# Kernel tuning notes

Hardware: AMD Instinct MI355X
Metric: run time of the kernel (lower is better)

## Reference

```python
import jax, jax.numpy as jnp
import numpy as np

B, H, S, D = 4, 16, 2048, 64
TEMPERATURE = 8.0  # sqrt(D)
MASK_FILL = -1e9


def setup_inputs() -> dict:
    key = jax.random.key(0)
    kq, kk, kv, km = jax.random.split(key, 4)
    q = jax.random.normal(kq, (B, H, S, D), dtype=jnp.float32)
    k = jax.random.normal(kk, (B, H, S, D), dtype=jnp.float32)
    v = jax.random.normal(kv, (B, H, S, D), dtype=jnp.float32)
    mask = jax.random.randint(km, (B, 1, 1, S), 0, 2, dtype=jnp.int32)
    return {"q": q, "k": k, "v": v, "mask": mask}


def reference(q, k, v, mask):
    # attn = (q / temperature) @ k^T  -> [B,H,S,S]
    attn = jnp.einsum('bhqd,bhkd->bhqk', q / TEMPERATURE, k)
    # mask-fill where mask == 0 (broadcasts over heads/query dim)
    attn = jnp.where(mask == 0, MASK_FILL, attn)
    # dropout is identity at inference (training=None in the original)
    # NOTE: the original module applies NO softmax; faithful reproduction.
    output = jnp.einsum('bhqk,bhkd->bhqd', attn, v)
    return (output, attn)
```

## Files before the change

kernel.cpp:

```cpp
#include <hip/hip_runtime.h>

constexpr int Bn = 4, Hn = 16, Sn = 2048, Dn = 64;
constexpr float MASK_FILL = -1e9f;

typedef __bf16 bf16x8 __attribute__((ext_vector_type(8)));
typedef __bf16 bf16x4 __attribute__((ext_vector_type(4)));
typedef float  f32x4  __attribute__((ext_vector_type(4)));

#define KSTRIDE 72
#define VSTRIDE 136

__global__ __launch_bounds__(256, 2) void attn_fused(
    const float* __restrict__ qg, const float* __restrict__ kg,
    const float* __restrict__ vg, const int* __restrict__ maskg,
    float* __restrict__ outg, float* __restrict__ attng)
{
  __shared__ __align__(16) __bf16 lds_k [128 * KSTRIDE];
  __shared__ __align__(16) __bf16 lds_vt[ 64 * VSTRIDE];
  __shared__ __align__(16) __bf16 lds_qs[128 * KSTRIDE];
  __shared__ int lds_m[128];

  const int qt   = blockIdx.x;
  const int bh   = blockIdx.y;
  const int b    = bh >> 4;
  const int tid  = threadIdx.x;
  const int wave = tid >> 6;
  const int lane = tid & 63;
  const int quad = lane >> 4;
  const int l16  = lane & 15;

  const size_t hbase = (size_t)bh * Sn * Dn;
  const float* qp = qg + hbase + (size_t)qt * 128 * Dn;
  float* attnp = attng + (size_t)bh * Sn * Sn + (size_t)qt * 128 * (size_t)Sn;

  {
    const int r0 = tid >> 4;
    const int c  = (tid & 15) << 2;
#pragma unroll
    for (int i = 0; i < 8; ++i) {
      const int r = r0 + (i << 4);
      f32x4 val = __builtin_nontemporal_load((const f32x4*)(qp + r * Dn + c));
      bf16x4 pk;
      pk.x = (__bf16)(val.x * 0.125f);
      pk.y = (__bf16)(val.y * 0.125f);
      pk.z = (__bf16)(val.z * 0.125f);
      pk.w = (__bf16)(val.w * 0.125f);
      *(bf16x4*)&lds_qs[r * KSTRIDE + c] = pk;
    }
  }
  __syncthreads();

  bf16x8 qa[2][2];
#pragma unroll
  for (int qs = 0; qs < 2; ++qs)
#pragma unroll
    for (int ks = 0; ks < 2; ++ks)
      qa[qs][ks] = *(const bf16x8*)&lds_qs[(wave * 32 + qs * 16 + l16) * KSTRIDE + ks * 32 + quad * 8];

  __bf16* sbuf = &lds_qs[wave * 32 * KSTRIDE];

  f32x4 oacc[2][4];
#pragma unroll
  for (int qs = 0; qs < 2; ++qs)
#pragma unroll
    for (int ds = 0; ds < 4; ++ds)
      oacc[qs][ds] = (f32x4){0.f, 0.f, 0.f, 0.f};

  for (int kt = 0; kt < 16; ++kt) {
    __syncthreads();

    {
      const int r0 = tid >> 4;
      const int c  = (tid & 15) << 2;
      const float* kp = kg + hbase + (size_t)(kt * 128) * Dn;
      const float* vp = vg + hbase + (size_t)(kt * 128) * Dn;
#pragma unroll
      for (int i = 0; i < 8; ++i) {
        const int r = r0 + (i << 4);
        f32x4 kv = *(const f32x4*)(kp + r * Dn + c);
        bf16x4 pk;
        pk.x = (__bf16)kv.x; pk.y = (__bf16)kv.y;
        pk.z = (__bf16)kv.z; pk.w = (__bf16)kv.w;
        *(bf16x4*)&lds_k[r * KSTRIDE + c] = pk;
        f32x4 vv = *(const f32x4*)(vp + r * Dn + c);
        lds_vt[(c + 0) * VSTRIDE + r] = (__bf16)vv.x;
        lds_vt[(c + 1) * VSTRIDE + r] = (__bf16)vv.y;
        lds_vt[(c + 2) * VSTRIDE + r] = (__bf16)vv.z;
        lds_vt[(c + 3) * VSTRIDE + r] = (__bf16)vv.w;
      }
      if (tid < 128) lds_m[tid] = maskg[b * Sn + kt * 128 + tid];
    }
    __syncthreads();

    f32x4 sacc[2][8];
#pragma unroll
    for (int ns = 0; ns < 8; ++ns) {
      bf16x8 kb0 = *(const bf16x8*)&lds_k[(ns * 16 + l16) * KSTRIDE +      quad * 8];
      bf16x8 kb1 = *(const bf16x8*)&lds_k[(ns * 16 + l16) * KSTRIDE + 32 + quad * 8];
#pragma unroll
      for (int qs = 0; qs < 2; ++qs) {
        f32x4 acc = (f32x4){0.f, 0.f, 0.f, 0.f};
        acc = __builtin_amdgcn_mfma_f32_16x16x32_bf16(qa[qs][0], kb0, acc, 0, 0, 0);
        acc = __builtin_amdgcn_mfma_f32_16x16x32_bf16(qa[qs][1], kb1, acc, 0, 0, 0);
        sacc[qs][ns] = acc;
      }
    }

#pragma unroll
    for (int ns = 0; ns < 8; ++ns) {
      const int col = ns * 16 + l16;
      const bool keep = (lds_m[col] != 0);
#pragma unroll
      for (int qs = 0; qs < 2; ++qs) {
#pragma unroll
        for (int rI = 0; rI < 4; ++rI) {
          float sv = keep ? sacc[qs][ns][rI] : MASK_FILL;
          sacc[qs][ns][rI] = sv;
          const int row = wave * 32 + qs * 16 + quad * 4 + rI;
          __builtin_nontemporal_store(sv, attnp + (size_t)row * Sn + kt * 128 + col);
        }
      }
    }

#pragma unroll
    for (int half = 0; half < 2; ++half) {
#pragma unroll
      for (int ns4 = 0; ns4 < 4; ++ns4) {
        const int ns = half * 4 + ns4;
#pragma unroll
        for (int qs = 0; qs < 2; ++qs)
#pragma unroll
          for (int rI = 0; rI < 4; ++rI)
            sbuf[(qs * 16 + quad * 4 + rI) * KSTRIDE + ns4 * 16 + l16] = (__bf16)sacc[qs][ns][rI];
      }
      asm volatile("" ::: "memory");
#pragma unroll
      for (int ks = 0; ks < 2; ++ks) {
        bf16x8 sa0 = *(const bf16x8*)&sbuf[(     l16) * KSTRIDE + ks * 32 + quad * 8];
        bf16x8 sa1 = *(const bf16x8*)&sbuf[(16 + l16) * KSTRIDE + ks * 32 + quad * 8];
#pragma unroll
        for (int ds = 0; ds < 4; ++ds) {
          bf16x8 vb = *(const bf16x8*)&lds_vt[(ds * 16 + l16) * VSTRIDE + half * 64 + ks * 32 + quad * 8];
          oacc[0][ds] = __builtin_amdgcn_mfma_f32_16x16x32_bf16(sa0, vb, oacc[0][ds], 0, 0, 0);
          oacc[1][ds] = __builtin_amdgcn_mfma_f32_16x16x32_bf16(sa1, vb, oacc[1][ds], 0, 0, 0);
        }
      }
      asm volatile("" ::: "memory");
    }
  }

  float* op = outg + hbase + (size_t)qt * 128 * Dn;
#pragma unroll
  for (int qs = 0; qs < 2; ++qs)
#pragma unroll
    for (int ds = 0; ds < 4; ++ds)
#pragma unroll
      for (int rI = 0; rI < 4; ++rI) {
        const int row = wave * 32 + qs * 16 + quad * 4 + rI;
        __builtin_nontemporal_store(oacc[qs][ds][rI], op + (size_t)row * Dn + ds * 16 + l16);
      }
}

extern "C" void kernel_launch(void* const* d_in, const int* in_sizes, int n_in,
                              void* d_out, int out_size, void* d_ws, size_t ws_size,
                              hipStream_t stream) {
  const float* q    = (const float*)d_in[0];
  const float* k    = (const float*)d_in[1];
  const float* v    = (const float*)d_in[2];
  const int*   mask = (const int*)d_in[3];
  float* out  = (float*)d_out;
  float* attn = out + (size_t)Bn * Hn * Sn * Dn;

  dim3 grid(Sn / 128, Bn * Hn);
  attn_fused<<<grid, 256, 0, stream>>>(q, k, v, mask, out, attn);
}
```

Baseline: 1.310 ms.

## Prefetch K/V into registers, transpose MFMA operands for vectorized stores, remap blocks

Loads the next K/V tile into registers while the current tile is computed, so global latency overlaps the MFMA work. Swaps the MFMA operand order so each lane holds four consecutive columns, which lets the attn and output writes use 16-byte vector stores instead of scalar ones. Loads the whole mask row into LDS once and remaps block indices to spread work across XCDs. This costs extra registers for the prefetch buffers and more LDS for the mask, which could reduce occupancy.

```diff
diff --git a/kernel.cpp b/kernel.cpp
--- a/kernel.cpp
+++ b/kernel.cpp
@@ -6,9 +6,12 @@
 typedef __bf16 bf16x8 __attribute__((ext_vector_type(8)));
 typedef __bf16 bf16x4 __attribute__((ext_vector_type(4)));
 typedef float  f32x4  __attribute__((ext_vector_type(4)));
+typedef int    i32x4  __attribute__((ext_vector_type(4)));
 
 #define KSTRIDE 72
 #define VSTRIDE 136
+
+#define BARRIER_LGKM() asm volatile("s_waitcnt lgkmcnt(0)\n\ts_barrier" ::: "memory")
 
 __global__ __launch_bounds__(256, 2) void attn_fused(
     const float* __restrict__ qg, const float* __restrict__ kg,
@@ -18,10 +21,12 @@
   __shared__ __align__(16) __bf16 lds_k [128 * KSTRIDE];
   __shared__ __align__(16) __bf16 lds_vt[ 64 * VSTRIDE];
   __shared__ __align__(16) __bf16 lds_qs[128 * KSTRIDE];
-  __shared__ int lds_m[128];
-
-  const int qt   = blockIdx.x;
-  const int bh   = blockIdx.y;
+  __shared__ __align__(16) int    lds_m [Sn];
+
+  const int fid  = blockIdx.y * gridDim.x + blockIdx.x;
+  const int nf   = ((fid & 7) << 7) | (fid >> 3);
+  const int qt   = nf & 15;
+  const int bh   = nf >> 4;
   const int b    = bh >> 4;
   const int tid  = threadIdx.x;
   const int wave = tid >> 6;
@@ -33,92 +38,114 @@
   const float* qp = qg + hbase + (size_t)qt * 128 * Dn;
   float* attnp = attng + (size_t)bh * Sn * Sn + (size_t)qt * 128 * (size_t)Sn;
 
+  const int r0 = tid >> 4;
+  const int c  = (tid & 15) << 2;
+
   {
-    const int r0 = tid >> 4;
-    const int c  = (tid & 15) << 2;
+    const int* mp = maskg + b * Sn;
+    *(i32x4*)&lds_m[tid * 8]     = *(const i32x4*)(mp + tid * 8);
+    *(i32x4*)&lds_m[tid * 8 + 4] = *(const i32x4*)(mp + tid * 8 + 4);
+  }
+
+#pragma unroll
+  for (int i = 0; i < 8; ++i) {
+    const int r = r0 + (i << 4);
+    f32x4 val = __builtin_nontemporal_load((const f32x4*)(qp + r * Dn + c));
+    bf16x4 pk;
+    pk.x = (__bf16)(val.x * 0.125f);
+    pk.y = (__bf16)(val.y * 0.125f);
+    pk.z = (__bf16)(val.z * 0.125f);
+    pk.w = (__bf16)(val.w * 0.125f);
+    *(bf16x4*)&lds_qs[r * KSTRIDE + c] = pk;
+  }
+
+  f32x4 kpre[8], vpre[8];
+  const float* kbase = kg + hbase;
+  const float* vbase = vg + hbase;
+#pragma unroll
+  for (int i = 0; i < 8; ++i) {
+    const int r = r0 + (i << 4);
+    kpre[i] = *(const f32x4*)(kbase + r * Dn + c);
+    vpre[i] = *(const f32x4*)(vbase + r * Dn + c);
+  }
+
+  BARRIER_LGKM();
+
+  bf16x8 qa[2][2];
+#pragma unroll
+  for (int qs = 0; qs < 2; ++qs)
+#pragma unroll
+    for (int ks = 0; ks < 2; ++ks)
+      qa[qs][ks] = *(const bf16x8*)&lds_qs[(wave * 32 + qs * 16 + l16) * KSTRIDE + ks * 32 + quad * 8];
+
+  __bf16* sbuf = &lds_qs[wave * 32 * KSTRIDE];
+
+  f32x4 oacc[2][4];
+#pragma unroll
+  for (int qs = 0; qs < 2; ++qs)
+#pragma unroll
+    for (int ds = 0; ds < 4; ++ds)
+      oacc[qs][ds] = (f32x4){0.f, 0.f, 0.f, 0.f};
+
+  for (int kt = 0; kt < 16; ++kt) {
+    BARRIER_LGKM();
+
 #pragma unroll
     for (int i = 0; i < 8; ++i) {
       const int r = r0 + (i << 4);
-      f32x4 val = __builtin_nontemporal_load((const f32x4*)(qp + r * Dn + c));
+      f32x4 kv = kpre[i];
       bf16x4 pk;
-      pk.x = (__bf16)(val.x * 0.125f);
-      pk.y = (__bf16)(val.y * 0.125f);
-      pk.z = (__bf16)(val.z * 0.125f);
-      pk.w = (__bf16)(val.w * 0.125f);
-      *(bf16x4*)&lds_qs[r * KSTRIDE + c] = pk;
-    }
-  }
-  __syncthreads();
-
-  bf16x8 qa[2][2];
-#pragma unroll
-  for (int qs = 0; qs < 2; ++qs)
-#pragma unroll
-    for (int ks = 0; ks < 2; ++ks)
-      qa[qs][ks] = *(const bf16x8*)&lds_qs[(wave * 32 + qs * 16 + l16) * KSTRIDE + ks * 32 + quad * 8];
-
-  __bf16* sbuf = &lds_qs[wave * 32 * KSTRIDE];
-
-  f32x4 oacc[2][4];
-#pragma unroll
-  for (int qs = 0; qs < 2; ++qs)
-#pragma unroll
-    for (int ds = 0; ds < 4; ++ds)
-      oacc[qs][ds] = (f32x4){0.f, 0.f, 0.f, 0.f};
-
-  for (int kt = 0; kt < 16; ++kt) {
-    __syncthreads();
-
-    {
-      const int r0 = tid >> 4;
-      const int c  = (tid & 15) << 2;
-      const float* kp = kg + hbase + (size_t)(kt * 128) * Dn;
-      const float* vp = vg + hbase + (size_t)(kt * 128) * Dn;
+      pk.x = (__bf16)kv.x; pk.y = (__bf16)kv.y;
+      pk.z = (__bf16)kv.z; pk.w = (__bf16)kv.w;
+      *(bf16x4*)&lds_k[r * KSTRIDE + c] = pk;
+      f32x4 vv = vpre[i];
+      lds_vt[(c + 0) * VSTRIDE + r] = (__bf16)vv.x;
+      lds_vt[(c + 1) * VSTRIDE + r] = (__bf16)vv.y;
+      lds_vt[(c + 2) * VSTRIDE + r] = (__bf16)vv.z;
+      lds_vt[(c + 3) * VSTRIDE + r] = (__bf16)vv.w;
+    }
+
+    BARRIER_LGKM();
+
+    if (kt < 15) {
+      const float* kp = kbase + (size_t)((kt + 1) * 128) * Dn;
+      const float* vp = vbase + (size_t)((kt + 1) * 128) * Dn;
 #pragma unroll
       for (int i = 0; i < 8; ++i) {
         const int r = r0 + (i << 4);
-        f32x4 kv = *(const f32x4*)(kp + r * Dn + c);
-        bf16x4 pk;
-        pk.x = (__bf16)kv.x; pk.y = (__bf16)kv.y;
-        pk.z = (__bf16)kv.z; pk.w = (__bf16)kv.w;
-        *(bf16x4*)&lds_k[r * KSTRIDE + c] = pk;
-        f32x4 vv = *(const f32x4*)(vp + r * Dn + c);
-        lds_vt[(c + 0) * VSTRIDE + r] = (__bf16)vv.x;
-        lds_vt[(c + 1) * VSTRIDE + r] = (__bf16)vv.y;
-        lds_vt[(c + 2) * VSTRIDE + r] = (__bf16)vv.z;
-        lds_vt[(c + 3) * VSTRIDE + r] = (__bf16)vv.w;
-      }
-      if (tid < 128) lds_m[tid] = maskg[b * Sn + kt * 128 + tid];
-    }
-    __syncthreads();
+        kpre[i] = *(const f32x4*)(kp + r * Dn + c);
+        vpre[i] = *(const f32x4*)(vp + r * Dn + c);
+      }
+    }
 
     f32x4 sacc[2][8];
 #pragma unroll
     for (int ns = 0; ns < 8; ++ns) {
-      bf16x8 kb0 = *(const bf16x8*)&lds_k[(ns * 16 + l16) * KSTRIDE +      quad * 8];
-      bf16x8 kb1 = *(const bf16x8*)&lds_k[(ns * 16 + l16) * KSTRIDE + 32 + quad * 8];
+      bf16x8 ka0 = *(const bf16x8*)&lds_k[(ns * 16 + l16) * KSTRIDE +      quad * 8];
+      bf16x8 ka1 = *(const bf16x8*)&lds_k[(ns * 16 + l16) * KSTRIDE + 32 + quad * 8];
 #pragma unroll
       for (int qs = 0; qs < 2; ++qs) {
         f32x4 acc = (f32x4){0.f, 0.f, 0.f, 0.f};
-        acc = __builtin_amdgcn_mfma_f32_16x16x32_bf16(qa[qs][0], kb0, acc, 0, 0, 0);
-        acc = __builtin_amdgcn_mfma_f32_16x16x32_bf16(qa[qs][1], kb1, acc, 0, 0, 0);
+        acc = __builtin_amdgcn_mfma_f32_16x16x32_bf16(ka0, qa[qs][0], acc, 0, 0, 0);
+        acc = __builtin_amdgcn_mfma_f32_16x16x32_bf16(ka1, qa[qs][1], acc, 0, 0, 0);
         sacc[qs][ns] = acc;
       }
     }
 
 #pragma unroll
     for (int ns = 0; ns < 8; ++ns) {
-      const int col = ns * 16 + l16;
-      const bool keep = (lds_m[col] != 0);
+      const i32x4 m4 = *(const i32x4*)&lds_m[kt * 128 + ns * 16 + quad * 4];
 #pragma unroll
       for (int qs = 0; qs < 2; ++qs) {
-#pragma unroll
-        for (int rI = 0; rI < 4; ++rI) {
-          float sv = keep ? sacc[qs][ns][rI] : MASK_FILL;
-          sacc[qs][ns][rI] = sv;
-          const int row = wave * 32 + qs * 16 + quad * 4 + rI;
-          __builtin_nontemporal_store(sv, attnp + (size_t)row * Sn + kt * 128 + col);
-        }
+        f32x4 sv = sacc[qs][ns];
+        sv.x = m4.x ? sv.x : MASK_FILL;
+        sv.y = m4.y ? sv.y : MASK_FILL;
+        sv.z = m4.z ? sv.z : MASK_FILL;
+        sv.w = m4.w ? sv.w : MASK_FILL;
+        sacc[qs][ns] = sv;
+        const int row = wave * 32 + qs * 16 + l16;
+        __builtin_nontemporal_store(sv,
+            (f32x4*)(attnp + (size_t)row * Sn + kt * 128 + ns * 16 + quad * 4));
       }
     }
 
@@ -128,21 +155,24 @@
       for (int ns4 = 0; ns4 < 4; ++ns4) {
         const int ns = half * 4 + ns4;
 #pragma unroll
-        for (int qs = 0; qs < 2; ++qs)
-#pragma unroll
-          for (int rI = 0; rI < 4; ++rI)
-            sbuf[(qs * 16 + quad * 4 + rI) * KSTRIDE + ns4 * 16 + l16] = (__bf16)sacc[qs][ns][rI];
+        for (int qs = 0; qs < 2; ++qs) {
+          f32x4 sv = sacc[qs][ns];
+          bf16x4 sb;
+          sb.x = (__bf16)sv.x; sb.y = (__bf16)sv.y;
+          sb.z = (__bf16)sv.z; sb.w = (__bf16)sv.w;
+          *(bf16x4*)&sbuf[(qs * 16 + l16) * KSTRIDE + ns4 * 16 + quad * 4] = sb;
+        }
       }
       asm volatile("" ::: "memory");
 #pragma unroll
       for (int ks = 0; ks < 2; ++ks) {
-        bf16x8 sa0 = *(const bf16x8*)&sbuf[(     l16) * KSTRIDE + ks * 32 + quad * 8];
-        bf16x8 sa1 = *(const bf16x8*)&sbuf[(16 + l16) * KSTRIDE + ks * 32 + quad * 8];
+        bf16x8 sb0 = *(const bf16x8*)&sbuf[(     l16) * KSTRIDE + ks * 32 + quad * 8];
+        bf16x8 sb1 = *(const bf16x8*)&sbuf[(16 + l16) * KSTRIDE + ks * 32 + quad * 8];
 #pragma unroll
         for (int ds = 0; ds < 4; ++ds) {
-          bf16x8 vb = *(const bf16x8*)&lds_vt[(ds * 16 + l16) * VSTRIDE + half * 64 + ks * 32 + quad * 8];
-          oacc[0][ds] = __builtin_amdgcn_mfma_f32_16x16x32_bf16(sa0, vb, oacc[0][ds], 0, 0, 0);
-          oacc[1][ds] = __builtin_amdgcn_mfma_f32_16x16x32_bf16(sa1, vb, oacc[1][ds], 0, 0, 0);
+          bf16x8 va = *(const bf16x8*)&lds_vt[(ds * 16 + l16) * VSTRIDE + half * 64 + ks * 32 + quad * 8];
+          oacc[0][ds] = __builtin_amdgcn_mfma_f32_16x16x32_bf16(va, sb0, oacc[0][ds], 0, 0, 0);
+          oacc[1][ds] = __builtin_amdgcn_mfma_f32_16x16x32_bf16(va, sb1, oacc[1][ds], 0, 0, 0);
         }
       }
       asm volatile("" ::: "memory");
@@ -153,12 +183,11 @@
 #pragma unroll
   for (int qs = 0; qs < 2; ++qs)
 #pragma unroll
-    for (int ds = 0; ds < 4; ++ds)
-#pragma unroll
-      for (int rI = 0; rI < 4; ++rI) {
-        const int row = wave * 32 + qs * 16 + quad * 4 + rI;
-        __builtin_nontemporal_store(oacc[qs][ds][rI], op + (size_t)row * Dn + ds * 16 + l16);
-      }
+    for (int ds = 0; ds < 4; ++ds) {
+      const int row = wave * 32 + qs * 16 + l16;
+      __builtin_nontemporal_store(oacc[qs][ds],
+          (f32x4*)(op + (size_t)row * Dn + ds * 16 + quad * 4));
+    }
 }
 
 extern "C" void kernel_launch(void* const* d_in, const int* in_sizes, int n_in,
```

Result: no change. 1.302 ms (-0.6%).
